# Optimization experiments

Hardware: AMD Instinct MI355X
Metric: run time of the kernel (lower is better)

Reference implementation:

```python
import jax, jax.numpy as jnp
import numpy as np

NEG_SLOPE = 0.2

def setup_inputs() -> dict:
    key = jax.random.key(0)
    k1, k2, k3 = jax.random.split(key, 3)
    B, C, H, W = 8, 256, 128, 128
    R = 16  # reduction -> squeeze dim C // R = 16
    Cs = C // R
    x = jax.random.normal(k1, (B, C, H, W), dtype=jnp.float32)
    w1 = jax.random.normal(k2, (Cs, C), dtype=jnp.float32) * (1.0 / np.sqrt(C))
    b1 = jnp.zeros((Cs,), dtype=jnp.float32)
    w2 = jax.random.normal(k3, (C, Cs), dtype=jnp.float32) * (1.0 / np.sqrt(Cs))
    b2 = jnp.zeros((C,), dtype=jnp.float32)
    return {"x": x, "w1": w1, "b1": b1, "w2": w2, "b2": b2}

def reference(x, w1, b1, w2, b2):
    # Global average pool over spatial dims: [B,C,H,W] -> [B,C]
    y = jnp.mean(x, axis=(2, 3))
    # 1x1 conv on [B,C,1,1] == GEMV: squeeze + LeakyReLU(0.2)
    y1 = jnp.einsum('bc,sc->bs', y, w1) + b1
    y1 = jnp.where(y1 >= 0, y1, NEG_SLOPE * y1)
    # excite + sigmoid gate
    y2 = jax.nn.sigmoid(jnp.einsum('bs,cs->bc', y1, w2) + b2)
    # broadcast channel-wise scale
    return x * y2[:, :, None, None]
```

## Files before the change

### kernel.cpp

```cpp
#include <hip/hip_runtime.h>
#include <math.h>

#define Bn 8
#define Cn 256
#define CSn 16
#define HWn 16384
#define PL4 4096
#define NEG_SLOPE 0.2f

typedef float f4v __attribute__((ext_vector_type(4)));

__global__ __launch_bounds__(256) void pool_kernel(const float* __restrict__ x,
                                                   float* __restrict__ y) {
    const int bc = blockIdx.x;
    const f4v* xp = (const f4v*)x + (size_t)bc * PL4;
    const int t = threadIdx.x;
    float sum = 0.f;
    #pragma unroll
    for (int i = 0; i < 16; ++i) {
        f4v v = xp[t + i * 256];
        sum += (v.x + v.y) + (v.z + v.w);
    }
    #pragma unroll
    for (int off = 32; off; off >>= 1)
        sum += __shfl_down(sum, off, 64);
    __shared__ float sm[4];
    if ((t & 63) == 0) sm[t >> 6] = sum;
    __syncthreads();
    if (t == 0)
        y[bc] = (sm[0] + sm[1] + sm[2] + sm[3]) * (1.f / (float)HWn);
}

__global__ __launch_bounds__(256) void scale_kernel(const float* __restrict__ x,
                                                    const float* __restrict__ y,
                                                    const float* __restrict__ w1,
                                                    const float* __restrict__ b1,
                                                    const float* __restrict__ w2,
                                                    const float* __restrict__ b2,
                                                    float* __restrict__ out) {
    const int bc = blockIdx.x;
    const int b = bc >> 8, c = bc & (Cn - 1);
    const int t = threadIdx.x;

    __shared__ float part[CSn * 17];
    __shared__ float y1s[CSn];
    __shared__ float gsh;
    {
        const int s = t >> 4, j = t & 15;
        const float* yb = y  + b * Cn + j * 16;
        const float* wr = w1 + s * Cn + j * 16;
        float p = 0.f;
        #pragma unroll
        for (int k = 0; k < 16; ++k) p += yb[k] * wr[k];
        part[s * 17 + j] = p;
    }
    __syncthreads();
    if (t < CSn) {
        float a = b1[t];
        #pragma unroll
        for (int j = 0; j < 16; ++j) a += part[t * 17 + j];
        y1s[t] = (a >= 0.f) ? a : NEG_SLOPE * a;
    }
    __syncthreads();
    if (t == 0) {
        float a = b2[c];
        #pragma unroll
        for (int s = 0; s < CSn; ++s) a += y1s[s] * w2[c * CSn + s];
        gsh = 1.f / (1.f + __expf(-a));
    }
    __syncthreads();
    const float g = gsh;

    const f4v* xp = (const f4v*)x + (size_t)bc * PL4;
    f4v* op = (f4v*)out + (size_t)bc * PL4;
    #pragma unroll
    for (int i = 0; i < 16; ++i) {
        f4v v = xp[t + i * 256];
        v *= g;
        __builtin_nontemporal_store(v, &op[t + i * 256]);
    }
}

extern "C" void kernel_launch(void* const* d_in, const int* in_sizes, int n_in,
                              void* d_out, int out_size, void* d_ws, size_t ws_size,
                              hipStream_t stream) {
    const float* x  = (const float*)d_in[0];
    const float* w1 = (const float*)d_in[1];
    const float* b1 = (const float*)d_in[2];
    const float* w2 = (const float*)d_in[3];
    const float* b2 = (const float*)d_in[4];
    float* out = (float*)d_out;
    float* y   = (float*)d_ws;

    pool_kernel<<<Bn * Cn, 256, 0, stream>>>(x, y);
    scale_kernel<<<Bn * Cn, 256, 0, stream>>>(x, y, w1, b1, w2, b2, out);
}
```

Measured before the change: 258.2 us.

## Compute SE gates once in last pool block; reverse plane order in scale pass

```diff
diff --git a/kernel.cpp b/kernel.cpp
--- a/kernel.cpp
+++ b/kernel.cpp
@@ -7,14 +7,24 @@
 #define HWn 16384
 #define PL4 4096
 #define NEG_SLOPE 0.2f
+#define NPLANES (Bn * Cn)
 
 typedef float f4v __attribute__((ext_vector_type(4)));
 
-__global__ __launch_bounds__(256) void pool_kernel(const float* __restrict__ x,
-                                                   float* __restrict__ y) {
+#define WS_Y_OFF 64
+#define WS_G_OFF (64 + NPLANES)
+
+__global__ __launch_bounds__(256) void pool_gate_kernel(
+    const float* __restrict__ x,  const float* __restrict__ w1,
+    const float* __restrict__ b1, const float* __restrict__ w2,
+    const float* __restrict__ b2, float* __restrict__ ws) {
+    float* y = ws + WS_Y_OFF;
+    float* g = ws + WS_G_OFF;
+    int*  cnt = (int*)ws;
     const int bc = blockIdx.x;
+    const int t  = threadIdx.x;
+
     const f4v* xp = (const f4v*)x + (size_t)bc * PL4;
-    const int t = threadIdx.x;
     float sum = 0.f;
     #pragma unroll
     for (int i = 0; i < 16; ++i) {
@@ -25,58 +35,66 @@
     for (int off = 32; off; off >>= 1)
         sum += __shfl_down(sum, off, 64);
     __shared__ float sm[4];
+    __shared__ int last;
     if ((t & 63) == 0) sm[t >> 6] = sum;
+    if (t == 0) last = 0;
     __syncthreads();
-    if (t == 0)
+    if (t == 0) {
         y[bc] = (sm[0] + sm[1] + sm[2] + sm[3]) * (1.f / (float)HWn);
+        __threadfence();
+        int old = atomicAdd(cnt, 1);
+        if (old == NPLANES - 1) last = 1;
+    }
+    __syncthreads();
+    if (!last) return;
+
+    __threadfence();
+    __shared__ float ys[NPLANES];
+    __shared__ float y1s[Bn * CSn];
+    #pragma unroll
+    for (int i = 0; i < NPLANES / 256; ++i)
+        ys[t + i * 256] = y[t + i * 256];
+    __syncthreads();
+    if (t < Bn * CSn) {
+        const int b = t >> 4, s = t & 15;
+        float acc = b1[s];
+        const float* wr = w1 + s * Cn;
+        #pragma unroll 8
+        for (int c = 0; c < Cn; ++c) acc += ys[b * Cn + c] * wr[c];
+        y1s[t] = (acc >= 0.f) ? acc : NEG_SLOPE * acc;
+    }
+    __syncthreads();
+    {
+        const int c = t;
+        const f4v* w2c = (const f4v*)(w2 + c * CSn);
+        f4v wv0 = w2c[0], wv1 = w2c[1], wv2 = w2c[2], wv3 = w2c[3];
+        const float bias = b2[c];
+        #pragma unroll
+        for (int b = 0; b < Bn; ++b) {
+            const float* yb = y1s + b * CSn;
+            float a = bias;
+            a += yb[0]*wv0.x + yb[1]*wv0.y + yb[2]*wv0.z + yb[3]*wv0.w;
+            a += yb[4]*wv1.x + yb[5]*wv1.y + yb[6]*wv1.z + yb[7]*wv1.w;
+            a += yb[8]*wv2.x + yb[9]*wv2.y + yb[10]*wv2.z + yb[11]*wv2.w;
+            a += yb[12]*wv3.x + yb[13]*wv3.y + yb[14]*wv3.z + yb[15]*wv3.w;
+            g[b * Cn + c] = 1.f / (1.f + __expf(-a));
+        }
+    }
 }
 
 __global__ __launch_bounds__(256) void scale_kernel(const float* __restrict__ x,
-                                                    const float* __restrict__ y,
-                                                    const float* __restrict__ w1,
-                                                    const float* __restrict__ b1,
-                                                    const float* __restrict__ w2,
-                                                    const float* __restrict__ b2,
+                                                    const float* __restrict__ ws,
                                                     float* __restrict__ out) {
-    const int bc = blockIdx.x;
-    const int b = bc >> 8, c = bc & (Cn - 1);
+    const int blk = blockIdx.x;
+    const int plane = (((NPLANES / 8 - 1) - (blk >> 3)) << 3) | (blk & 7);
+    const float gval = ws[WS_G_OFF + plane];
     const int t = threadIdx.x;
-
-    __shared__ float part[CSn * 17];
-    __shared__ float y1s[CSn];
-    __shared__ float gsh;
-    {
-        const int s = t >> 4, j = t & 15;
-        const float* yb = y  + b * Cn + j * 16;
-        const float* wr = w1 + s * Cn + j * 16;
-        float p = 0.f;
-        #pragma unroll
-        for (int k = 0; k < 16; ++k) p += yb[k] * wr[k];
-        part[s * 17 + j] = p;
-    }
-    __syncthreads();
-    if (t < CSn) {
-        float a = b1[t];
-        #pragma unroll
-        for (int j = 0; j < 16; ++j) a += part[t * 17 + j];
-        y1s[t] = (a >= 0.f) ? a : NEG_SLOPE * a;
-    }
-    __syncthreads();
-    if (t == 0) {
-        float a = b2[c];
-        #pragma unroll
-        for (int s = 0; s < CSn; ++s) a += y1s[s] * w2[c * CSn + s];
-        gsh = 1.f / (1.f + __expf(-a));
-    }
-    __syncthreads();
-    const float g = gsh;
-
-    const f4v* xp = (const f4v*)x + (size_t)bc * PL4;
-    f4v* op = (f4v*)out + (size_t)bc * PL4;
+    const f4v* xp = (const f4v*)x + (size_t)plane * PL4;
+    f4v* op = (f4v*)out + (size_t)plane * PL4;
     #pragma unroll
     for (int i = 0; i < 16; ++i) {
         f4v v = xp[t + i * 256];
-        v *= g;
+        v *= gval;
         __builtin_nontemporal_store(v, &op[t + i * 256]);
     }
 }
@@ -90,8 +108,9 @@
     const float* w2 = (const float*)d_in[3];
     const float* b2 = (const float*)d_in[4];
     float* out = (float*)d_out;
-    float* y   = (float*)d_ws;
+    float* ws  = (float*)d_ws;
 
-    pool_kernel<<<Bn * Cn, 256, 0, stream>>>(x, y);
-    scale_kernel<<<Bn * Cn, 256, 0, stream>>>(x, y, w1, b1, w2, b2, out);
+    hipMemsetAsync(d_ws, 0, 4, stream);
+    pool_gate_kernel<<<NPLANES, 256, 0, stream>>>(x, w1, b1, w2, b2, ws);
+    scale_kernel<<<NPLANES, 256, 0, stream>>>(x, ws, out);
 }
```

Result: slower. 360.7 us (+39.7%).
